# Optimization experiments

Hardware: AMD Instinct MI355X
Metric: run time of the kernel (lower is better)

Reference implementation:

```python
import jax, jax.numpy as jnp
import numpy as np

B, N, F, P, E, T = 8, 10000, 8, 12, 160000, 64
C = 32  # A3TGCN2 out_channels fixed to 32 in the module


def setup_inputs() -> dict:
    key = jax.random.key(0)
    ks = jax.random.split(key, 20)
    x = jax.random.normal(ks[0], (B, N, F, P), jnp.float32)
    edge_index = jax.random.randint(ks[1], (2, E), 0, N, dtype=jnp.int64)
    edge_weight = jax.random.uniform(ks[2], (E,), jnp.float32)

    def g(k, shape):
        return jax.random.normal(k, shape, jnp.float32) * 0.05

    return dict(
        x=x, edge_index=edge_index, edge_weight=edge_weight,
        Wz=g(ks[3], (F, C)), bz=g(ks[4], (C,)),
        Wr=g(ks[5], (F, C)), br=g(ks[6], (C,)),
        Wh=g(ks[7], (F, C)), bh=g(ks[8], (C,)),
        Lz_w=g(ks[9], (2 * C, C)), Lz_b=g(ks[10], (C,)),
        Lr_w=g(ks[11], (2 * C, C)), Lr_b=g(ks[12], (C,)),
        Lh_w=g(ks[13], (2 * C, C)), Lh_b=g(ks[14], (C,)),
        att=g(ks[15], (P,)),
        lin1_w=g(ks[16], (C, P)), lin1_b=g(ks[17], (P,)),
        lin2_w=g(ks[18], (N, T)), lin2_b=g(ks[19], (T,)),
    )


def _gcn_norm(edge_index, edge_weight, n):
    # GCNConv default: add self-loops (weight 1) + symmetric normalization
    row, col = edge_index[0], edge_index[1]
    loop = jnp.arange(n)
    row = jnp.concatenate([row, loop])
    col = jnp.concatenate([col, loop])
    w = jnp.concatenate([edge_weight, jnp.ones((n,), edge_weight.dtype)])
    deg = jax.ops.segment_sum(w, col, num_segments=n)
    dis = jnp.where(deg > 0, jax.lax.rsqrt(jnp.where(deg > 0, deg, 1.0)), 0.0)
    return row, col, dis[row] * w * dis[col]


def _gcn_conv(X, W, b, row, col, norm, n):
    XW = X @ W                                   # [B,N,C]
    msg = XW[:, row, :] * norm[None, :, None]    # gather over source nodes
    out = jnp.zeros((X.shape[0], n, W.shape[1]), X.dtype).at[:, col, :].add(msg)
    return out + b


def reference(x, edge_index, edge_weight, Wz, bz, Wr, br, Wh, bh,
              Lz_w, Lz_b, Lr_w, Lr_b, Lh_w, Lh_b, att,
              lin1_w, lin1_b, lin2_w, lin2_b):
    b_, n, _, periods = x.shape
    row, col, norm = _gcn_norm(edge_index, edge_weight, n)
    probs = jax.nn.softmax(att)
    # A3TGCN2 passes H=None to the TGCN cell at every period -> hidden state
    # is zeros for every period (faithful to library implementation).
    H0 = jnp.zeros((b_, n, Lz_w.shape[1]), x.dtype)
    H_accum = jnp.zeros_like(H0)
    for p in range(periods):
        Xp = x[:, :, :, p]                       # [B,N,F]
        Z = jax.nn.sigmoid(
            jnp.concatenate([_gcn_conv(Xp, Wz, bz, row, col, norm, n), H0], axis=2) @ Lz_w + Lz_b)
        R = jax.nn.sigmoid(
            jnp.concatenate([_gcn_conv(Xp, Wr, br, row, col, norm, n), H0], axis=2) @ Lr_w + Lr_b)
        Ht = jnp.tanh(
            jnp.concatenate([_gcn_conv(Xp, Wh, bh, row, col, norm, n), H0 * R], axis=2) @ Lh_w + Lh_b)
        H = Z * H0 + (1.0 - Z) * Ht
        H_accum = H_accum + probs[p] * H
    h = jax.nn.relu(H_accum)                     # [B,N,32]
    h = h @ lin1_w + lin1_b                      # [B,N,P]
    h = jnp.swapaxes(h, 2, 1)                    # [B,P,N]
    h = h @ lin2_w + lin2_b                      # [B,P,T]
    return jnp.swapaxes(h, 2, 1)                 # [B,T,P]
```

## Files before the change

### kernel.cpp

```cpp
#include <hip/hip_runtime.h>
#include <stdint.h>

#define NN 10000
#define NNP 10016
#define NB 8
#define NP 12
#define NT 64
#define NC 32
#define BCAP 64
#define FCN 80
#define FCH 125
#define XFB 1875

typedef float v2f __attribute__((ext_vector_type(2)));

__device__ __forceinline__ v2f sp(float v) { v2f r; r.x = v; r.y = v; return r; }

__global__ __launch_bounds__(256) void k_pre(
    const float* __restrict__ x, unsigned char* __restrict__ xq,
    int* __restrict__ zbase,
    const float* __restrict__ Wz, const float* __restrict__ bz,
    const float* __restrict__ Wh, const float* __restrict__ bh,
    const float* __restrict__ Lzw, const float* __restrict__ Lzb,
    const float* __restrict__ Lhw, const float* __restrict__ Lhb,
    const float* __restrict__ att, float* __restrict__ sm) {
    const int blk = blockIdx.x, tid = threadIdx.x;
    if (blk < XFB) {
        const int gid = blk * 256 + tid;
        const int s0 = gid * 2;
        const int b = s0 / 120000, rem = s0 - b * 120000;
        const int n = rem / 12, q0 = rem - n * 12;
        const int pr = b >> 1, sb = b & 1;
        const float* px = x + (size_t)b * 960000 + n * 96 + q0 * 8;
        unsigned char* pw = xq + ((size_t)(pr * NNP + n) * 192) + sb * 96 + q0 * 8;
        const float4 f0 = *(const float4*)px;
        const float4 f1 = *(const float4*)(px + 4);
        const float4 f2 = *(const float4*)(px + 8);
        const float4 f3 = *(const float4*)(px + 12);
        int u0 = __builtin_amdgcn_cvt_pk_fp8_f32(f0.x, f0.y, 0, false);
        u0     = __builtin_amdgcn_cvt_pk_fp8_f32(f0.z, f0.w, u0, true);
        int u1 = __builtin_amdgcn_cvt_pk_fp8_f32(f1.x, f1.y, 0, false);
        u1     = __builtin_amdgcn_cvt_pk_fp8_f32(f1.z, f1.w, u1, true);
        int u2 = __builtin_amdgcn_cvt_pk_fp8_f32(f2.x, f2.y, 0, false);
        u2     = __builtin_amdgcn_cvt_pk_fp8_f32(f2.z, f2.w, u2, true);
        int u3 = __builtin_amdgcn_cvt_pk_fp8_f32(f3.x, f3.y, 0, false);
        u3     = __builtin_amdgcn_cvt_pk_fp8_f32(f3.z, f3.w, u3, true);
        *(uint4*)pw = make_uint4((unsigned)u0, (unsigned)u1, (unsigned)u2, (unsigned)u3);
    } else if (blk < XFB + 20) {
        const int i = (blk - XFB) * 256 + tid;
        *(int4*)(zbase + i * 4) = make_int4(0, 0, 0, 0);
    } else {
        const int t = tid, f = t >> 5, c = t & 31;
        float mz = 0.f, mh = 0.f;
        for (int j = 0; j < NC; ++j) {
            mz += Wz[f * NC + j] * Lzw[j * NC + c];
            mh += Wh[f * NC + j] * Lhw[j * NC + c];
        }
        sm[16 + 2 * t]     = mz;
        sm[16 + 2 * t + 1] = mh;
        if (t < NC) {
            float cz = Lzb[t], ch = Lhb[t];
            for (int j = 0; j < NC; ++j) {
                cz += bz[j] * Lzw[j * NC + t];
                ch += bh[j] * Lhw[j * NC + t];
            }
            sm[528 + 2 * t]     = cz;
            sm[528 + 2 * t + 1] = ch;
        }
        if (t == 0) {
            float m = -1e30f;
            for (int p = 0; p < NP; ++p) m = fmaxf(m, att[p]);
            float e[NP]; float s = 0.f;
            for (int p = 0; p < NP; ++p) { e[p] = __expf(att[p] - m); s += e[p]; }
            for (int p = 0; p < NP; ++p) sm[p] = e[p] / s;
        }
    }
}

__global__ __launch_bounds__(256) void k_edge(const int* __restrict__ rowp, const int* __restrict__ colp,
                                              const float* __restrict__ ew,
                                              float* __restrict__ deg, int* __restrict__ count,
                                              uint2* __restrict__ bucket, int E) {
    const int e = blockIdx.x * 256 + threadIdx.x;
    if (e < E) {
        const int c = colp[e];
        const float w = ew[e];
        atomicAdd(&deg[c], w);
        const int slot = atomicAdd(&count[c], 1);
        if (slot < BCAP) bucket[slot * NN + c] = make_uint2((unsigned)rowp[e], __float_as_uint(w));
    }
}

__global__ __launch_bounds__(256) void k_nrm(const float* __restrict__ deg, const int* __restrict__ count,
                                             uint2* __restrict__ bucket) {
    const int n = blockIdx.x * 256 + threadIdx.x;
    const int slot = blockIdx.y;
    if (n < NN && slot < min(count[n], BCAP)) {
        const uint2 e = bucket[slot * NN + n];
        const float nrm = rsqrtf(deg[e.x] + 1.0f) * __uint_as_float(e.y) * rsqrtf(deg[n] + 1.0f);
        bucket[slot * NN + n] = make_uint2(e.x * 192u, __float_as_uint(nrm));
    }
}

#define DEC3(U0, U1, U2, ACC, W)                                                        \
    ACC[0] = __builtin_elementwise_fma((v2f)__builtin_amdgcn_cvt_pk_f32_fp8((int)(U0), false), W, ACC[0]); \
    ACC[1] = __builtin_elementwise_fma((v2f)__builtin_amdgcn_cvt_pk_f32_fp8((int)(U0), true),  W, ACC[1]); \
    ACC[2] = __builtin_elementwise_fma((v2f)__builtin_amdgcn_cvt_pk_f32_fp8((int)(U1), false), W, ACC[2]); \
    ACC[3] = __builtin_elementwise_fma((v2f)__builtin_amdgcn_cvt_pk_f32_fp8((int)(U1), true),  W, ACC[3]); \
    ACC[4] = __builtin_elementwise_fma((v2f)__builtin_amdgcn_cvt_pk_f32_fp8((int)(U2), false), W, ACC[4]); \
    ACC[5] = __builtin_elementwise_fma((v2f)__builtin_amdgcn_cvt_pk_f32_fp8((int)(U2), true),  W, ACC[5])

__global__ __launch_bounds__(64, 2) void k_main(
    const unsigned char* __restrict__ xq, const float* __restrict__ deg,
    const int* __restrict__ count, const uint2* __restrict__ bucket,
    const float* __restrict__ sm,
    const float* __restrict__ l1w, const float* __restrict__ l1b,
    float* __restrict__ h1t) {
    __shared__ float sY[16][100];
    __shared__ float sHA[16 * 33];

    const int l = threadIdx.x;
    const int pr = blockIdx.x & 3;
    const int unit = blockIdx.x >> 2;
    const int g = l >> 3, j8 = l & 7;
    const int n = unit * 8 + g;
    const char* xb = (const char*)xq + (size_t)pr * NNP * 192;
    const unsigned lo12 = (unsigned)j8 * 12u;

    const int cnt = min(count[n], BCAP);
    v2f A[6], B[6];
    {
        const float dn = rsqrtf(deg[n] + 1.0f);
        const v2f vsn = sp(dn * dn);
        const char* p0 = xb + ((unsigned)n * 192u + lo12);
        const unsigned u0 = *(const unsigned*)p0;
        const unsigned u1 = *(const unsigned*)(p0 + 4);
        const unsigned u2 = *(const unsigned*)(p0 + 8);
        const unsigned v0 = *(const unsigned*)(p0 + 96);
        const unsigned v1 = *(const unsigned*)(p0 + 100);
        const unsigned v2_ = *(const unsigned*)(p0 + 104);
        A[0] = (v2f)__builtin_amdgcn_cvt_pk_f32_fp8((int)u0, false) * vsn;
        A[1] = (v2f)__builtin_amdgcn_cvt_pk_f32_fp8((int)u0, true)  * vsn;
        A[2] = (v2f)__builtin_amdgcn_cvt_pk_f32_fp8((int)u1, false) * vsn;
        A[3] = (v2f)__builtin_amdgcn_cvt_pk_f32_fp8((int)u1, true)  * vsn;
        A[4] = (v2f)__builtin_amdgcn_cvt_pk_f32_fp8((int)u2, false) * vsn;
        A[5] = (v2f)__builtin_amdgcn_cvt_pk_f32_fp8((int)u2, true)  * vsn;
        B[0] = (v2f)__builtin_amdgcn_cvt_pk_f32_fp8((int)v0, false) * vsn;
        B[1] = (v2f)__builtin_amdgcn_cvt_pk_f32_fp8((int)v0, true)  * vsn;
        B[2] = (v2f)__builtin_amdgcn_cvt_pk_f32_fp8((int)v1, false) * vsn;
        B[3] = (v2f)__builtin_amdgcn_cvt_pk_f32_fp8((int)v1, true)  * vsn;
        B[4] = (v2f)__builtin_amdgcn_cvt_pk_f32_fp8((int)v2_, false) * vsn;
        B[5] = (v2f)__builtin_amdgcn_cvt_pk_f32_fp8((int)v2_, true)  * vsn;
    }

    int mcnt = cnt;
    #pragma unroll
    for (int off = 1; off < 64; off <<= 1) mcnt = max(mcnt, __shfl_xor(mcnt, off));

    for (int base = 0; base < mcnt; base += 8) {
        unsigned ex = 0u, ey = 0u;
        const int e = base + j8;
        if (e < cnt) {
            const uint2 be = bucket[e * NN + n];
            ex = be.x;
            ey = be.y;
        }
        unsigned U[48];
        float    W8[8];
        #pragma unroll
        for (int j = 0; j < 8; ++j) {
            const int srcl = g * 8 + j;
            const unsigned e2x = (unsigned)__shfl((int)ex, srcl);
            W8[j] = __uint_as_float((unsigned)__shfl((int)ey, srcl));
            const char* p = xb + (e2x + lo12);
            U[j * 6 + 0] = *(const unsigned*)p;
            U[j * 6 + 1] = *(const unsigned*)(p + 4);
            U[j * 6 + 2] = *(const unsigned*)(p + 8);
            U[j * 6 + 3] = *(const unsigned*)(p + 96);
            U[j * 6 + 4] = *(const unsigned*)(p + 100);
            U[j * 6 + 5] = *(const unsigned*)(p + 104);
        }
        #pragma unroll
        for (int j = 0; j < 8; ++j) {
            const v2f w = sp(W8[j]);
            DEC3(U[j * 6 + 0], U[j * 6 + 1], U[j * 6 + 2], A, w);
            DEC3(U[j * 6 + 3], U[j * 6 + 4], U[j * 6 + 5], B, w);
        }
    }
    {
        float* ya = &sY[g * 2 + 0][j8 * 12];
        float* yb2 = &sY[g * 2 + 1][j8 * 12];
        *(float4*)ya       = make_float4(A[0].x, A[0].y, A[1].x, A[1].y);
        *(float4*)(ya + 4) = make_float4(A[2].x, A[2].y, A[3].x, A[3].y);
        *(float4*)(ya + 8) = make_float4(A[4].x, A[4].y, A[5].x, A[5].y);
        *(float4*)yb2       = make_float4(B[0].x, B[0].y, B[1].x, B[1].y);
        *(float4*)(yb2 + 4) = make_float4(B[2].x, B[2].y, B[3].x, B[3].y);
        *(float4*)(yb2 + 8) = make_float4(B[4].x, B[4].y, B[5].x, B[5].y);
    }

    const int c = l & 31;
    const float2* __restrict__ smzh = (const float2*)(sm + 16);
    const float2* __restrict__ sczh = (const float2*)(sm + 528);
    v2f m8[8];
    #pragma unroll
    for (int f = 0; f < 8; ++f) { const float2 t2 = smzh[f * 32 + c]; v2f v; v.x = t2.x; v.y = t2.y; m8[f] = v; }
    v2f czh;
    { const float2 t2 = sczh[c]; czh.x = t2.x; czh.y = t2.y; }
    float pr12[12];
    #pragma unroll
    for (int p = 0; p < 12; ++p) pr12[p] = sm[p];

    #pragma unroll
    for (int t8 = 0; t8 < 8; ++t8) {
        const int r = t8 * 2 + (l >> 5);
        const float* yb = &sY[r][0];
        v2f zh[12];
        #pragma unroll
        for (int p = 0; p < 12; ++p) zh[p] = czh;
        #pragma unroll
        for (int f = 0; f < 8; ++f) {
            const float4 y0 = *(const float4*)(yb + f * 12);
            const float4 y1 = *(const float4*)(yb + f * 12 + 4);
            const float4 y2 = *(const float4*)(yb + f * 12 + 8);
            const v2f mm = m8[f];
            zh[0]  = __builtin_elementwise_fma(sp(y0.x), mm, zh[0]);
            zh[1]  = __builtin_elementwise_fma(sp(y0.y), mm, zh[1]);
            zh[2]  = __builtin_elementwise_fma(sp(y0.z), mm, zh[2]);
            zh[3]  = __builtin_elementwise_fma(sp(y0.w), mm, zh[3]);
            zh[4]  = __builtin_elementwise_fma(sp(y1.x), mm, zh[4]);
            zh[5]  = __builtin_elementwise_fma(sp(y1.y), mm, zh[5]);
            zh[6]  = __builtin_elementwise_fma(sp(y1.z), mm, zh[6]);
            zh[7]  = __builtin_elementwise_fma(sp(y1.w), mm, zh[7]);
            zh[8]  = __builtin_elementwise_fma(sp(y2.x), mm, zh[8]);
            zh[9]  = __builtin_elementwise_fma(sp(y2.y), mm, zh[9]);
            zh[10] = __builtin_elementwise_fma(sp(y2.z), mm, zh[10]);
            zh[11] = __builtin_elementwise_fma(sp(y2.w), mm, zh[11]);
        }
        float hacc = 0.f;
        #pragma unroll
        for (int p = 0; p < 12; ++p) {
            const float u = __expf(-zh[p].x);
            const float v = __expf(2.f * zh[p].y);
            const float num = u * (v - 1.f);
            const float den = fmaf(u, v, u) + (v + 1.f);
            hacc = fmaf(pr12[p] * num, __builtin_amdgcn_rcpf(den), hacc);
        }
        sHA[r * 33 + c] = fmaxf(hacc, 0.f);
    }

    #pragma unroll
    for (int tt = 0; tt < 3; ++tt) {
        const int task = l + tt * 64;
        const int r = task / 12, p = task - r * 12;
        const int nn = unit * 8 + (r >> 1);
        if (nn < NN) {
            float s = l1b[p];
            #pragma unroll
            for (int cc = 0; cc < 32; ++cc) s = fmaf(sHA[r * 33 + cc], l1w[cc * 12 + p], s);
            h1t[nn * 96 + (pr * 2 + (r & 1)) * 12 + p] = s;
        }
    }
}

__global__ __launch_bounds__(256) void k_final(const float* __restrict__ h1t, const float* __restrict__ W2,
                                               float* __restrict__ partial) {
    __shared__ float sh1[96 * FCN];
    const int tid = threadIdx.x;
    const int n0 = blockIdx.x * FCN;

    for (int idx = tid; idx < 96 * FCN; idx += 256) {
        const int nn = idx / 96, i = idx - nn * 96;
        sh1[i * FCN + nn] = h1t[(n0 + nn) * 96 + i];
    }
    __syncthreads();

    const int t = tid & 63, w = tid >> 6;
    const float* sh = &sh1[w * 24 * FCN];
    float acc[24];
    #pragma unroll
    for (int j = 0; j < 24; ++j) acc[j] = 0.f;

    for (int nn = 0; nn < FCN; nn += 4) {
        const float w20 = W2[(n0 + nn + 0) * NT + t];
        const float w21 = W2[(n0 + nn + 1) * NT + t];
        const float w22 = W2[(n0 + nn + 2) * NT + t];
        const float w23 = W2[(n0 + nn + 3) * NT + t];
        #pragma unroll
        for (int j = 0; j < 24; ++j) {
            const float4 hv = *(const float4*)&sh[j * FCN + nn];
            acc[j] = fmaf(hv.x, w20, fmaf(hv.y, w21, fmaf(hv.z, w22, fmaf(hv.w, w23, acc[j]))));
        }
    }

    float* pp = partial + blockIdx.x * 6144 + w * 24 * 64 + t;
    #pragma unroll
    for (int j = 0; j < 24; ++j) pp[j * 64] = acc[j];
}

__global__ __launch_bounds__(256) void k_red(const float* __restrict__ partial, const float* __restrict__ l2b,
                                             float* __restrict__ out) {
    __shared__ float red[4][64];
    const int i = blockIdx.x;
    const int t = threadIdx.x & 63, g = threadIdx.x >> 6;
    float s = 0.f;
    for (int c = g; c < FCH; c += 4)
        s += partial[c * 6144 + i * 64 + t];
    red[g][t] = s;
    __syncthreads();
    if (g == 0) {
        const float v = red[0][t] + red[1][t] + red[2][t] + red[3][t] + l2b[t];
        const int b = i / 12, p = i - b * 12;
        out[b * 768 + t * 12 + p] = v;
    }
}

extern "C" void kernel_launch(void* const* d_in, const int* in_sizes, int n_in,
                              void* d_out, int out_size, void* d_ws, size_t ws_size,
                              hipStream_t stream) {
    const float* x    = (const float*)d_in[0];
    const int*   eidx = (const int*)d_in[1];
    const float* ew   = (const float*)d_in[2];
    const float* Wz   = (const float*)d_in[3];
    const float* bz   = (const float*)d_in[4];
    const float* Wh   = (const float*)d_in[7];
    const float* bh   = (const float*)d_in[8];
    const float* Lzw  = (const float*)d_in[9];
    const float* Lzb  = (const float*)d_in[10];
    const float* Lhw  = (const float*)d_in[13];
    const float* Lhb  = (const float*)d_in[14];
    const float* att  = (const float*)d_in[15];
    const float* l1w  = (const float*)d_in[16];
    const float* l1b  = (const float*)d_in[17];
    const float* W2   = (const float*)d_in[18];
    const float* l2b  = (const float*)d_in[19];
    float* out = (float*)d_out;
    const int E = in_sizes[2];
    const int EB = (E + 255) / 256;

    float* deg    = (float*)d_ws;
    int*   count  = (int*)(deg + 10240);
    uint2* bucket = (uint2*)(count + 10240);
    float* sm     = (float*)(bucket + NN * BCAP);
    float* h1t    = sm + 1024;
    unsigned char* xq = (unsigned char*)(h1t + NN * 96);
    float* partial = (float*)(xq + (size_t)4 * NNP * 192);

    const int* rowp = eidx;
    const int* colp = eidx + E;

    hipLaunchKernelGGL(k_pre, dim3(XFB + 21), dim3(256), 0, stream,
                       x, xq, (int*)d_ws, Wz, bz, Wh, bh, Lzw, Lzb, Lhw, Lhb, att, sm);
    hipLaunchKernelGGL(k_edge, dim3(EB), dim3(256), 0, stream, rowp, colp, ew, deg, count, bucket, E);
    hipLaunchKernelGGL(k_nrm, dim3(40, BCAP), dim3(256), 0, stream, deg, count, bucket);
    hipLaunchKernelGGL(k_main, dim3(1252 * 4), dim3(64), 0, stream,
                       xq, deg, count, bucket, sm, l1w, l1b, h1t);
    hipLaunchKernelGGL(k_final, dim3(FCH), dim3(256), 0, stream, h1t, W2, partial);
    hipLaunchKernelGGL(k_red, dim3(96), dim3(256), 0, stream, partial, l2b, out);
}
```

Before: 108.4 us.

## Fuse all stages into one persistent cooperative kernel with grid syncs

Replaces the six-kernel launch sequence with a single cooperative persistent kernel that runs each stage (quantize/precompute, edge bucketing, normalization, main gather/GRU, final linear, reduction) in grid-stride loops separated by grid.sync(). This removes inter-kernel launch gaps and tail effects. In exchange, every stage now runs on a fixed grid of at most 2048 blocks of 128 threads, grid-wide barriers add their own cost, and the main stage's work distribution changes to two waves per block. The original multi-kernel path is kept as a fallback if the cooperative launch fails.

```diff
diff --git a/kernel.cpp b/kernel.cpp
--- a/kernel.cpp
+++ b/kernel.cpp
@@ -1,20 +1,306 @@
 #include <hip/hip_runtime.h>
+#include <hip/hip_cooperative_groups.h>
 #include <stdint.h>
+
+namespace cg = cooperative_groups;
 
 #define NN 10000
 #define NNP 10016
-#define NB 8
 #define NP 12
 #define NT 64
 #define NC 32
 #define BCAP 64
 #define FCN 80
 #define FCH 125
+#define BLK 128
 #define XFB 1875
 
 typedef float v2f __attribute__((ext_vector_type(2)));
-
 __device__ __forceinline__ v2f sp(float v) { v2f r; r.x = v; r.y = v; return r; }
+
+#define DEC3(U0, U1, U2, ACC, W)                                                        \
+    ACC[0] = __builtin_elementwise_fma((v2f)__builtin_amdgcn_cvt_pk_f32_fp8((int)(U0), false), W, ACC[0]); \
+    ACC[1] = __builtin_elementwise_fma((v2f)__builtin_amdgcn_cvt_pk_f32_fp8((int)(U0), true),  W, ACC[1]); \
+    ACC[2] = __builtin_elementwise_fma((v2f)__builtin_amdgcn_cvt_pk_f32_fp8((int)(U1), false), W, ACC[2]); \
+    ACC[3] = __builtin_elementwise_fma((v2f)__builtin_amdgcn_cvt_pk_f32_fp8((int)(U1), true),  W, ACC[3]); \
+    ACC[4] = __builtin_elementwise_fma((v2f)__builtin_amdgcn_cvt_pk_f32_fp8((int)(U2), false), W, ACC[4]); \
+    ACC[5] = __builtin_elementwise_fma((v2f)__builtin_amdgcn_cvt_pk_f32_fp8((int)(U2), true),  W, ACC[5])
+
+struct KArgs {
+    const float* x; const int* rowp; const int* colp; const float* ew;
+    const float* Wz; const float* bz; const float* Wh; const float* bh;
+    const float* Lzw; const float* Lzb; const float* Lhw; const float* Lhb;
+    const float* att; const float* l1w; const float* l1b; const float* W2; const float* l2b;
+    float* out; float* deg; int* count; uint2* bucket; float* sm; float* h1t;
+    unsigned char* xq; float* partial; int E;
+};
+
+__global__ __launch_bounds__(BLK, 2) void k_all(KArgs a) {
+    __shared__ union {
+        struct { float sY[2][16][100]; float sHA[2][528]; } m;
+        float sh1[48 * FCN];
+    } S;
+
+    cg::grid_group grid = cg::this_grid();
+    const int tid = threadIdx.x;
+    const int GS = gridDim.x * BLK;
+    const int gtid = blockIdx.x * BLK + tid;
+
+    for (int i = gtid; i < 5120; i += GS)
+        ((int4*)a.deg)[i] = make_int4(0, 0, 0, 0);
+    for (int gid = gtid; gid < 480000; gid += GS) {
+        const int s0 = gid * 2;
+        const int b = s0 / 120000, rem = s0 - b * 120000;
+        const int n = rem / 12, q0 = rem - n * 12;
+        const int pr = b >> 1, sb = b & 1;
+        const float* px = a.x + (size_t)b * 960000 + n * 96 + q0 * 8;
+        unsigned char* pw = a.xq + ((size_t)(pr * NNP + n) * 192) + sb * 96 + q0 * 8;
+        const float4 f0 = *(const float4*)px;
+        const float4 f1 = *(const float4*)(px + 4);
+        const float4 f2 = *(const float4*)(px + 8);
+        const float4 f3 = *(const float4*)(px + 12);
+        int u0 = __builtin_amdgcn_cvt_pk_fp8_f32(f0.x, f0.y, 0, false);
+        u0     = __builtin_amdgcn_cvt_pk_fp8_f32(f0.z, f0.w, u0, true);
+        int u1 = __builtin_amdgcn_cvt_pk_fp8_f32(f1.x, f1.y, 0, false);
+        u1     = __builtin_amdgcn_cvt_pk_fp8_f32(f1.z, f1.w, u1, true);
+        int u2 = __builtin_amdgcn_cvt_pk_fp8_f32(f2.x, f2.y, 0, false);
+        u2     = __builtin_amdgcn_cvt_pk_fp8_f32(f2.z, f2.w, u2, true);
+        int u3 = __builtin_amdgcn_cvt_pk_fp8_f32(f3.x, f3.y, 0, false);
+        u3     = __builtin_amdgcn_cvt_pk_fp8_f32(f3.z, f3.w, u3, true);
+        *(uint4*)pw = make_uint4((unsigned)u0, (unsigned)u1, (unsigned)u2, (unsigned)u3);
+    }
+    if (blockIdx.x == 0) {
+        for (int t = tid; t < 256; t += BLK) {
+            const int f = t >> 5, c = t & 31;
+            float mz = 0.f, mh = 0.f;
+            for (int j = 0; j < NC; ++j) {
+                mz += a.Wz[f * NC + j] * a.Lzw[j * NC + c];
+                mh += a.Wh[f * NC + j] * a.Lhw[j * NC + c];
+            }
+            a.sm[16 + 2 * t]     = mz;
+            a.sm[16 + 2 * t + 1] = mh;
+            if (t < NC) {
+                float cz = a.Lzb[t], ch = a.Lhb[t];
+                for (int j = 0; j < NC; ++j) {
+                    cz += a.bz[j] * a.Lzw[j * NC + t];
+                    ch += a.bh[j] * a.Lhw[j * NC + t];
+                }
+                a.sm[528 + 2 * t]     = cz;
+                a.sm[528 + 2 * t + 1] = ch;
+            }
+        }
+        if (tid == 0) {
+            float m = -1e30f;
+            for (int p = 0; p < NP; ++p) m = fmaxf(m, a.att[p]);
+            float e[NP]; float s = 0.f;
+            for (int p = 0; p < NP; ++p) { e[p] = __expf(a.att[p] - m); s += e[p]; }
+            for (int p = 0; p < NP; ++p) a.sm[p] = e[p] / s;
+        }
+    }
+    grid.sync();
+
+    for (int e = gtid; e < a.E; e += GS) {
+        const int c = a.colp[e];
+        const float w = a.ew[e];
+        atomicAdd(&a.deg[c], w);
+        const int slot = atomicAdd(&a.count[c], 1);
+        if (slot < BCAP) a.bucket[slot * NN + c] = make_uint2((unsigned)a.rowp[e], __float_as_uint(w));
+    }
+    grid.sync();
+
+    for (int i = gtid; i < BCAP * NN; i += GS) {
+        const int slot = i / NN, n = i - slot * NN;
+        if (slot < min(a.count[n], BCAP)) {
+            const uint2 e = a.bucket[i];
+            const float nrm = rsqrtf(a.deg[e.x] + 1.0f) * __uint_as_float(e.y) * rsqrtf(a.deg[n] + 1.0f);
+            a.bucket[i] = make_uint2(e.x * 192u, __float_as_uint(nrm));
+        }
+    }
+    grid.sync();
+
+    {
+        const int w = tid >> 6, l = tid & 63;
+        const int pr = blockIdx.x & 3;
+        const int bg = blockIdx.x >> 2;
+        const int bpp = gridDim.x >> 2;
+        const int g = l >> 3, j8 = l & 7;
+        const char* xb = (const char*)a.xq + (size_t)pr * NNP * 192;
+        const unsigned lo12 = (unsigned)j8 * 12u;
+        const int c = l & 31;
+        const float2* __restrict__ smzh = (const float2*)(a.sm + 16);
+        const float2* __restrict__ sczh = (const float2*)(a.sm + 528);
+        v2f m8[8];
+        #pragma unroll
+        for (int f = 0; f < 8; ++f) { const float2 t2 = smzh[f * 32 + c]; v2f v; v.x = t2.x; v.y = t2.y; m8[f] = v; }
+        v2f czh;
+        { const float2 t2 = sczh[c]; czh.x = t2.x; czh.y = t2.y; }
+        float pr12[NP];
+        #pragma unroll
+        for (int p = 0; p < NP; ++p) pr12[p] = a.sm[p];
+
+        for (int unit = w * bpp + bg; unit < 1252; unit += 2 * bpp) {
+            const int n = unit * 8 + g;
+            const int cnt = min(a.count[n], BCAP);
+            v2f A[6], B[6];
+            {
+                const float dn = rsqrtf(a.deg[n] + 1.0f);
+                const v2f vsn = sp(dn * dn);
+                const char* p0 = xb + ((unsigned)n * 192u + lo12);
+                const unsigned u0 = *(const unsigned*)p0;
+                const unsigned u1 = *(const unsigned*)(p0 + 4);
+                const unsigned u2 = *(const unsigned*)(p0 + 8);
+                const unsigned v0 = *(const unsigned*)(p0 + 96);
+                const unsigned v1 = *(const unsigned*)(p0 + 100);
+                const unsigned v2_ = *(const unsigned*)(p0 + 104);
+                A[0] = (v2f)__builtin_amdgcn_cvt_pk_f32_fp8((int)u0, false) * vsn;
+                A[1] = (v2f)__builtin_amdgcn_cvt_pk_f32_fp8((int)u0, true)  * vsn;
+                A[2] = (v2f)__builtin_amdgcn_cvt_pk_f32_fp8((int)u1, false) * vsn;
+                A[3] = (v2f)__builtin_amdgcn_cvt_pk_f32_fp8((int)u1, true)  * vsn;
+                A[4] = (v2f)__builtin_amdgcn_cvt_pk_f32_fp8((int)u2, false) * vsn;
+                A[5] = (v2f)__builtin_amdgcn_cvt_pk_f32_fp8((int)u2, true)  * vsn;
+                B[0] = (v2f)__builtin_amdgcn_cvt_pk_f32_fp8((int)v0, false) * vsn;
+                B[1] = (v2f)__builtin_amdgcn_cvt_pk_f32_fp8((int)v0, true)  * vsn;
+                B[2] = (v2f)__builtin_amdgcn_cvt_pk_f32_fp8((int)v1, false) * vsn;
+                B[3] = (v2f)__builtin_amdgcn_cvt_pk_f32_fp8((int)v1, true)  * vsn;
+                B[4] = (v2f)__builtin_amdgcn_cvt_pk_f32_fp8((int)v2_, false) * vsn;
+                B[5] = (v2f)__builtin_amdgcn_cvt_pk_f32_fp8((int)v2_, true)  * vsn;
+            }
+            int mcnt = cnt;
+            #pragma unroll
+            for (int off = 1; off < 64; off <<= 1) mcnt = max(mcnt, __shfl_xor(mcnt, off));
+
+            for (int base = 0; base < mcnt; base += 8) {
+                unsigned ex = 0u, ey = 0u;
+                const int e = base + j8;
+                if (e < cnt) {
+                    const uint2 be = a.bucket[e * NN + n];
+                    ex = be.x; ey = be.y;
+                }
+                unsigned U[48];
+                float    W8[8];
+                #pragma unroll
+                for (int j = 0; j < 8; ++j) {
+                    const int srcl = g * 8 + j;
+                    const unsigned e2x = (unsigned)__shfl((int)ex, srcl);
+                    W8[j] = __uint_as_float((unsigned)__shfl((int)ey, srcl));
+                    const char* p = xb + (e2x + lo12);
+                    U[j * 6 + 0] = *(const unsigned*)p;
+                    U[j * 6 + 1] = *(const unsigned*)(p + 4);
+                    U[j * 6 + 2] = *(const unsigned*)(p + 8);
+                    U[j * 6 + 3] = *(const unsigned*)(p + 96);
+                    U[j * 6 + 4] = *(const unsigned*)(p + 100);
+                    U[j * 6 + 5] = *(const unsigned*)(p + 104);
+                }
+                #pragma unroll
+                for (int j = 0; j < 8; ++j) {
+                    const v2f wv = sp(W8[j]);
+                    DEC3(U[j * 6 + 0], U[j * 6 + 1], U[j * 6 + 2], A, wv);
+                    DEC3(U[j * 6 + 3], U[j * 6 + 4], U[j * 6 + 5], B, wv);
+                }
+            }
+            {
+                float* ya = &S.m.sY[w][g * 2 + 0][j8 * 12];
+                float* yb2 = &S.m.sY[w][g * 2 + 1][j8 * 12];
+                *(float4*)ya       = make_float4(A[0].x, A[0].y, A[1].x, A[1].y);
+                *(float4*)(ya + 4) = make_float4(A[2].x, A[2].y, A[3].x, A[3].y);
+                *(float4*)(ya + 8) = make_float4(A[4].x, A[4].y, A[5].x, A[5].y);
+                *(float4*)yb2       = make_float4(B[0].x, B[0].y, B[1].x, B[1].y);
+                *(float4*)(yb2 + 4) = make_float4(B[2].x, B[2].y, B[3].x, B[3].y);
+                *(float4*)(yb2 + 8) = make_float4(B[4].x, B[4].y, B[5].x, B[5].y);
+            }
+            #pragma unroll
+            for (int t8 = 0; t8 < 8; ++t8) {
+                const int r = t8 * 2 + (l >> 5);
+                const float* yb = &S.m.sY[w][r][0];
+                v2f zh[NP];
+                #pragma unroll
+                for (int p = 0; p < NP; ++p) zh[p] = czh;
+                #pragma unroll
+                for (int f = 0; f < 8; ++f) {
+                    const float4 y0 = *(const float4*)(yb + f * 12);
+                    const float4 y1 = *(const float4*)(yb + f * 12 + 4);
+                    const float4 y2 = *(const float4*)(yb + f * 12 + 8);
+                    const v2f mm = m8[f];
+                    zh[0]  = __builtin_elementwise_fma(sp(y0.x), mm, zh[0]);
+                    zh[1]  = __builtin_elementwise_fma(sp(y0.y), mm, zh[1]);
+                    zh[2]  = __builtin_elementwise_fma(sp(y0.z), mm, zh[2]);
+                    zh[3]  = __builtin_elementwise_fma(sp(y0.w), mm, zh[3]);
+                    zh[4]  = __builtin_elementwise_fma(sp(y1.x), mm, zh[4]);
+                    zh[5]  = __builtin_elementwise_fma(sp(y1.y), mm, zh[5]);
+                    zh[6]  = __builtin_elementwise_fma(sp(y1.z), mm, zh[6]);
+                    zh[7]  = __builtin_elementwise_fma(sp(y1.w), mm, zh[7]);
+                    zh[8]  = __builtin_elementwise_fma(sp(y2.x), mm, zh[8]);
+                    zh[9]  = __builtin_elementwise_fma(sp(y2.y), mm, zh[9]);
+                    zh[10] = __builtin_elementwise_fma(sp(y2.z), mm, zh[10]);
+                    zh[11] = __builtin_elementwise_fma(sp(y2.w), mm, zh[11]);
+                }
+                float hacc = 0.f;
+                #pragma unroll
+                for (int p = 0; p < NP; ++p) {
+                    const float u = __expf(-zh[p].x);
+                    const float v = __expf(2.f * zh[p].y);
+                    const float num = u * (v - 1.f);
+                    const float den = fmaf(u, v, u) + (v + 1.f);
+                    hacc = fmaf(pr12[p] * num, __builtin_amdgcn_rcpf(den), hacc);
+                }
+                S.m.sHA[w][r * 33 + c] = fmaxf(hacc, 0.f);
+            }
+            #pragma unroll
+            for (int tt = 0; tt < 3; ++tt) {
+                const int task = l + tt * 64;
+                const int r = task / 12, p = task - r * 12;
+                const int nn = unit * 8 + (r >> 1);
+                if (nn < NN) {
+                    float s = a.l1b[p];
+                    #pragma unroll
+                    for (int cc = 0; cc < 32; ++cc) s = fmaf(S.m.sHA[w][r * 33 + cc], a.l1w[cc * 12 + p], s);
+                    a.h1t[nn * 96 + (pr * 2 + (r & 1)) * 12 + p] = s;
+                }
+            }
+        }
+    }
+    grid.sync();
+
+    if (blockIdx.x < 250) {
+        const int chunk = blockIdx.x >> 1, h = blockIdx.x & 1;
+        const int n0 = chunk * FCN, i0 = h * 48;
+        for (int idx = tid; idx < 48 * FCN; idx += BLK) {
+            const int nn = idx / 48, i = idx - nn * 48;
+            S.sh1[i * FCN + nn] = a.h1t[(n0 + nn) * 96 + i0 + i];
+        }
+        __syncthreads();
+        const int t = tid & 63, w = tid >> 6;
+        const float* sh = &S.sh1[w * 24 * FCN];
+        float acc[24];
+        #pragma unroll
+        for (int j = 0; j < 24; ++j) acc[j] = 0.f;
+        for (int nn = 0; nn < FCN; nn += 4) {
+            const float w20 = a.W2[(n0 + nn + 0) * NT + t];
+            const float w21 = a.W2[(n0 + nn + 1) * NT + t];
+            const float w22 = a.W2[(n0 + nn + 2) * NT + t];
+            const float w23 = a.W2[(n0 + nn + 3) * NT + t];
+            #pragma unroll
+            for (int j = 0; j < 24; ++j) {
+                const float4 hv = *(const float4*)&S.sh1[(w * 24 + j) * FCN + nn];
+                acc[j] = fmaf(hv.x, w20, fmaf(hv.y, w21, fmaf(hv.z, w22, fmaf(hv.w, w23, acc[j]))));
+            }
+            (void)sh;
+        }
+        float* pp = a.partial + chunk * 6144 + (i0 + w * 24) * 64 + t;
+        #pragma unroll
+        for (int j = 0; j < 24; ++j) pp[j * 64] = acc[j];
+    }
+    grid.sync();
+
+    if (blockIdx.x < 48) {
+        const int idx = blockIdx.x * BLK + tid;
+        const int i = idx >> 6, t = idx & 63;
+        float s = a.l2b[t];
+        for (int cch = 0; cch < FCH; ++cch) s += a.partial[cch * 6144 + idx];
+        const int b = i / 12, p = i - b * 12;
+        a.out[b * 768 + t * 12 + p] = s;
+    }
+}
 
 __global__ __launch_bounds__(256) void k_pre(
     const float* __restrict__ x, unsigned char* __restrict__ xq,
@@ -102,14 +388,6 @@
     }
 }
 
-#define DEC3(U0, U1, U2, ACC, W)                                                        \
-    ACC[0] = __builtin_elementwise_fma((v2f)__builtin_amdgcn_cvt_pk_f32_fp8((int)(U0), false), W, ACC[0]); \
-    ACC[1] = __builtin_elementwise_fma((v2f)__builtin_amdgcn_cvt_pk_f32_fp8((int)(U0), true),  W, ACC[1]); \
-    ACC[2] = __builtin_elementwise_fma((v2f)__builtin_amdgcn_cvt_pk_f32_fp8((int)(U1), false), W, ACC[2]); \
-    ACC[3] = __builtin_elementwise_fma((v2f)__builtin_amdgcn_cvt_pk_f32_fp8((int)(U1), true),  W, ACC[3]); \
-    ACC[4] = __builtin_elementwise_fma((v2f)__builtin_amdgcn_cvt_pk_f32_fp8((int)(U2), false), W, ACC[4]); \
-    ACC[5] = __builtin_elementwise_fma((v2f)__builtin_amdgcn_cvt_pk_f32_fp8((int)(U2), true),  W, ACC[5])
-
 __global__ __launch_bounds__(64, 2) void k_main(
     const unsigned char* __restrict__ xq, const float* __restrict__ deg,
     const int* __restrict__ count, const uint2* __restrict__ bucket,
@@ -348,12 +626,34 @@
     const int* rowp = eidx;
     const int* colp = eidx + E;
 
-    hipLaunchKernelGGL(k_pre, dim3(XFB + 21), dim3(256), 0, stream,
-                       x, xq, (int*)d_ws, Wz, bz, Wh, bh, Lzw, Lzb, Lhw, Lhb, att, sm);
-    hipLaunchKernelGGL(k_edge, dim3(EB), dim3(256), 0, stream, rowp, colp, ew, deg, count, bucket, E);
-    hipLaunchKernelGGL(k_nrm, dim3(40, BCAP), dim3(256), 0, stream, deg, count, bucket);
-    hipLaunchKernelGGL(k_main, dim3(1252 * 4), dim3(64), 0, stream,
-                       xq, deg, count, bucket, sm, l1w, l1b, h1t);
-    hipLaunchKernelGGL(k_final, dim3(FCH), dim3(256), 0, stream, h1t, W2, partial);
-    hipLaunchKernelGGL(k_red, dim3(96), dim3(256), 0, stream, partial, l2b, out);
-}
+    KArgs args;
+    args.x = x; args.rowp = rowp; args.colp = colp; args.ew = ew;
+    args.Wz = Wz; args.bz = bz; args.Wh = Wh; args.bh = bh;
+    args.Lzw = Lzw; args.Lzb = Lzb; args.Lhw = Lhw; args.Lhb = Lhb;
+    args.att = att; args.l1w = l1w; args.l1b = l1b; args.W2 = W2; args.l2b = l2b;
+    args.out = out; args.deg = deg; args.count = count; args.bucket = bucket;
+    args.sm = sm; args.h1t = h1t; args.xq = xq; args.partial = partial; args.E = E;
+
+    bool coop_ok = false;
+    int occ = 0;
+    if (hipOccupancyMaxActiveBlocksPerMultiprocessor(&occ, k_all, BLK, 0) == hipSuccess && occ > 0) {
+        int grid = occ * 256;
+        if (grid > 2048) grid = 2048;
+        grid &= ~3;
+        if (grid >= 256) {
+            void* params[] = { &args };
+            coop_ok = (hipLaunchCooperativeKernel(reinterpret_cast<void*>(k_all), dim3(grid), dim3(BLK),
+                                                  params, 0, stream) == hipSuccess);
+        }
+    }
+    if (!coop_ok) {
+        hipLaunchKernelGGL(k_pre, dim3(XFB + 21), dim3(256), 0, stream,
+                           x, xq, (int*)d_ws, Wz, bz, Wh, bh, Lzw, Lzb, Lhw, Lhb, att, sm);
+        hipLaunchKernelGGL(k_edge, dim3(EB), dim3(256), 0, stream, rowp, colp, ew, deg, count, bucket, E);
+        hipLaunchKernelGGL(k_nrm, dim3(40, BCAP), dim3(256), 0, stream, deg, count, bucket);
+        hipLaunchKernelGGL(k_main, dim3(1252 * 4), dim3(64), 0, stream,
+                           xq, deg, count, bucket, sm, l1w, l1b, h1t);
+        hipLaunchKernelGGL(k_final, dim3(FCH), dim3(256), 0, stream, h1t, W2, partial);
+        hipLaunchKernelGGL(k_red, dim3(96), dim3(256), 0, stream, partial, l2b, out);
+    }
+}
```

Measured after the change: 415.2 us. 3.83x slower.
